# Optimization experiments

Hardware: AMD Instinct MI355X
Metric: run time of the kernel (lower is better)

The kernel has to match this reference:

```python
import jax, jax.numpy as jnp
import numpy as np

B, N, C, H, W = 4, 24, 256, 100, 100
SCALE = 0.25      # feature-map stride scale (MultiScaleRoIAlign spatial scale)
OUT = 7           # output_size
SR = 2            # sampling_ratio
IMG = H / SCALE   # image size in box coordinates (400)


def setup_inputs() -> dict:
    key = jax.random.key(0)
    kf, kx, ky, kw, kh = jax.random.split(key, 5)
    features = jax.random.normal(kf, (B, C, H, W), dtype=jnp.float32)
    # valid boxes: positive height/width (module asserts non-degenerate boxes)
    x1 = jax.random.uniform(kx, (B, N), minval=0.0, maxval=IMG * 0.6)
    y1 = jax.random.uniform(ky, (B, N), minval=0.0, maxval=IMG * 0.6)
    bw = jax.random.uniform(kw, (B, N), minval=16.0, maxval=IMG * 0.35)
    bh = jax.random.uniform(kh, (B, N), minval=16.0, maxval=IMG * 0.35)
    x2 = jnp.minimum(x1 + bw, IMG - 1.0)
    y2 = jnp.minimum(y1 + bh, IMG - 1.0)
    boxes = jnp.stack([x1, y1, x2, y2], axis=-1)  # [B, N, 4] xyxy
    return {"features": features, "boxes": boxes}


def _roi_align(features, rois, batch_ix):
    """torchvision-style RoIAlign (aligned=False). rois: [R,4] xyxy in image coords."""
    R = rois.shape[0]
    x1, y1, x2, y2 = [rois[:, i] * SCALE for i in range(4)]
    roi_w = jnp.maximum(x2 - x1, 1.0)
    roi_h = jnp.maximum(y2 - y1, 1.0)
    bin_w = roi_w / OUT
    bin_h = roi_h / OUT
    # sample-point offsets within the roi: (bin + (k+0.5)/SR) for k in [0,SR)
    grid = (jnp.arange(OUT, dtype=jnp.float32)[:, None]
            + (jnp.arange(SR, dtype=jnp.float32)[None, :] + 0.5) / SR).reshape(-1)  # [OUT*SR]
    ys = y1[:, None] + grid[None, :] * bin_h[:, None]  # [R, 14]
    xs = x1[:, None] + grid[None, :] * bin_w[:, None]  # [R, 14]
    Y = ys[:, :, None]  # [R,14,1]
    X = xs[:, None, :]  # [R,1,14]
    valid = (Y > -1.0) & (Y < H) & (X > -1.0) & (X < W)  # [R,14,14]
    Yc = jnp.clip(Y, 0.0, H - 1.0)
    Xc = jnp.clip(X, 0.0, W - 1.0)
    y0f = jnp.floor(Yc); x0f = jnp.floor(Xc)
    ly = Yc - y0f; lx = Xc - x0f
    hy = 1.0 - ly;  hx = 1.0 - lx
    y0 = y0f.astype(jnp.int32); x0 = x0f.astype(jnp.int32)
    y1i = jnp.minimum(y0 + 1, H - 1); x1i = jnp.minimum(x0 + 1, W - 1)
    b = batch_ix[:, None, None]
    # gathers -> [R,14,14,C] each (advanced indices around the ':' put C last)
    f00 = features[b, :, y0,  x0]
    f01 = features[b, :, y0,  x1i]
    f10 = features[b, :, y1i, x0]
    f11 = features[b, :, y1i, x1i]
    w00 = (hy * hx)[..., None]; w01 = (hy * lx)[..., None]
    w10 = (ly * hx)[..., None]; w11 = (ly * lx)[..., None]
    val = (w00 * f00 + w01 * f01 + w10 * f10 + w11 * f11) * valid[..., None]
    # average SRxSR samples per bin -> [R, OUT, OUT, C] -> [R, C, OUT, OUT]
    pooled = val.reshape(R, OUT, SR, OUT, SR, C).mean(axis=(2, 4))
    return pooled.transpose(0, 3, 1, 2)


def reference(features, boxes):
    # 1) pairwise union boxes (vectorized form of _single_image_expand)
    iu, ju = jnp.triu_indices(N, k=1)          # P pairs, i<j
    b1 = boxes[:, iu]                          # [B, P, 4]
    b2 = boxes[:, ju]
    union = jnp.concatenate([jnp.minimum(b1[..., :2], b2[..., :2]),
                             jnp.maximum(b1[..., 2:], b2[..., 2:])], axis=-1)
    rois = jnp.concatenate([boxes, union], axis=1)  # [B, M, 4], M = N + P
    M = rois.shape[1]
    batch_ix = jnp.repeat(jnp.arange(B), M)
    pooled = _roi_align(features, rois.reshape(-1, 4), batch_ix)  # [B*M, C, 7, 7]
    pooled = pooled.reshape(B, M, C, OUT, OUT)
    # 2) pair assembly (vectorized _ObjPairLayer): [obj_i, obj_j, union_ij]
    obj = pooled[:, :N]    # [B, N, C, 7, 7]
    uni = pooled[:, N:]    # [B, P, C, 7, 7]
    pair_feats = jnp.stack([obj[:, iu], obj[:, ju], uni], axis=2)  # [B, P, 3, C, 7, 7]
    P = iu.shape[0]
    return pair_feats.reshape(B * P, 3, C, OUT, OUT)
```

## Files before the change

### kernel.cpp

```cpp
#include <hip/hip_runtime.h>

#define B_    4
#define N_OBJ 24
#define C_    256
#define H_    100
#define W_    100
#define HW_   (H_ * W_)
#define OUT_  7
#define P_    276
#define M_    (N_OBJ + P_)
#define SCALE_ 0.25f
#define CHW_OUT (C_ * OUT_ * OUT_)

typedef float f4_t __attribute__((ext_vector_type(4)));

__global__ __launch_bounds__(256) void transpose_kernel(
        const float* __restrict__ feat, float* __restrict__ featT) {
    __shared__ float tile[64][65];
    const int b   = blockIdx.z;
    const int c0  = blockIdx.y * 64;
    const int px0 = blockIdx.x * 64;
    const int t   = threadIdx.x;
    const int cl  = t >> 6;
    const int px  = t & 63;
#pragma unroll
    for (int k = 0; k < 16; ++k) {
        const int c_loc = cl + k * 4;
        const int gpx   = px0 + px;
        tile[c_loc][px] = (gpx < HW_)
            ? feat[((size_t)b * C_ + c0 + c_loc) * HW_ + gpx] : 0.0f;
    }
    __syncthreads();
    const int c2 = t & 63;
    const int pl = t >> 6;
#pragma unroll
    for (int k = 0; k < 16; ++k) {
        const int px_l = pl + k * 4;
        const int gpx  = px0 + px_l;
        if (gpx < HW_)
            featT[((size_t)b * HW_ + gpx) * C_ + c0 + c2] = tile[c2][px_l];
    }
}

__global__ __launch_bounds__(256) void roi_fused_kernel(
        const float* __restrict__ featT,
        const float* __restrict__ boxes,
        float* __restrict__ out) {
    __shared__ float lds[CHW_OUT];
    const int blk    = blockIdx.x;
    const bool is_obj = blk < B_ * N_OBJ;
    int b, m;
    if (is_obj) {
        b = (blk & 7) >> 1;
        m = ((blk >> 3) << 1) | (blk & 1);
    } else {
        const int t = blk - B_ * N_OBJ;
        b = (t & 7) >> 1;
        m = N_OBJ + (((t >> 3) << 1) | (t & 1));
    }

    float x1, y1, x2, y2;
    if (is_obj) {
        const float* bp = boxes + ((size_t)b * N_OBJ + m) * 4;
        x1 = bp[0]; y1 = bp[1]; x2 = bp[2]; y2 = bp[3];
    } else {
        int p = m - N_OBJ;
        int ii = 0, rem = p;
        while (rem >= N_OBJ - 1 - ii) { rem -= (N_OBJ - 1 - ii); ++ii; }
        const int jj = ii + 1 + rem;
        const float* b1 = boxes + ((size_t)b * N_OBJ + ii) * 4;
        const float* b2 = boxes + ((size_t)b * N_OBJ + jj) * 4;
        x1 = fminf(b1[0], b2[0]); y1 = fminf(b1[1], b2[1]);
        x2 = fmaxf(b1[2], b2[2]); y2 = fmaxf(b1[3], b2[3]);
    }
    x1 *= SCALE_; y1 *= SCALE_; x2 *= SCALE_; y2 *= SCALE_;
    const float bin_w = fmaxf(x2 - x1, 1.0f) * (1.0f / OUT_);
    const float bin_h = fmaxf(y2 - y1, 1.0f) * (1.0f / OUT_);

    const int lane = threadIdx.x & 63;
    const int wv   = threadIdx.x >> 6;
    const f4_t* fbase = (const f4_t*)(featT + (size_t)b * HW_ * C_) + lane;

    for (int s = wv; s < OUT_ * OUT_; s += 4) {
        const int ph = s / OUT_, pw = s - ph * OUT_;

        int ri_[4]; float rw_[4];
        {
            const float Ya = y1 + ((float)ph + 0.25f) * bin_h;
            const float Yb = y1 + ((float)ph + 0.75f) * bin_h;
            const float va = (Ya > -1.0f && Ya < (float)H_) ? 1.0f : 0.0f;
            const float vb = (Yb > -1.0f && Yb < (float)H_) ? 1.0f : 0.0f;
            const float Yca = fminf(fmaxf(Ya, 0.0f), (float)(H_ - 1));
            const float Ycb = fminf(fmaxf(Yb, 0.0f), (float)(H_ - 1));
            const int y0a = (int)floorf(Yca);
            const int y0b = (int)floorf(Ycb);
            const float lya = Yca - (float)y0a;
            const float lyb = Ycb - (float)y0b;
            ri_[0] = y0a; ri_[1] = min(y0a + 1, H_ - 1);
            ri_[2] = y0b; ri_[3] = min(y0b + 1, H_ - 1);
            rw_[0] = va * (1.0f - lya); rw_[1] = va * lya;
            rw_[2] = vb * (1.0f - lyb); rw_[3] = vb * lyb;
            if (ri_[1] == ri_[0]) { rw_[0] += rw_[1]; rw_[1] = 0.0f; }
            if (ri_[3] == ri_[2]) { rw_[2] += rw_[3]; rw_[3] = 0.0f; }
            if (ri_[2] == ri_[0]) {
                rw_[0] += rw_[2]; rw_[1] += rw_[3]; rw_[2] = 0.0f; rw_[3] = 0.0f;
            } else if (ri_[2] == ri_[1]) {
                rw_[1] += rw_[2]; rw_[2] = 0.0f;
            }
        }
        int ci_[4]; float cw_[4];
        {
            const float Xa = x1 + ((float)pw + 0.25f) * bin_w;
            const float Xb = x1 + ((float)pw + 0.75f) * bin_w;
            const float va = (Xa > -1.0f && Xa < (float)W_) ? 0.25f : 0.0f;
            const float vb = (Xb > -1.0f && Xb < (float)W_) ? 0.25f : 0.0f;
            const float Xca = fminf(fmaxf(Xa, 0.0f), (float)(W_ - 1));
            const float Xcb = fminf(fmaxf(Xb, 0.0f), (float)(W_ - 1));
            const int x0a = (int)floorf(Xca);
            const int x0b = (int)floorf(Xcb);
            const float lxa = Xca - (float)x0a;
            const float lxb = Xcb - (float)x0b;
            ci_[0] = x0a; ci_[1] = min(x0a + 1, W_ - 1);
            ci_[2] = x0b; ci_[3] = min(x0b + 1, W_ - 1);
            cw_[0] = va * (1.0f - lxa); cw_[1] = va * lxa;
            cw_[2] = vb * (1.0f - lxb); cw_[3] = vb * lxb;
            if (ci_[1] == ci_[0]) { cw_[0] += cw_[1]; cw_[1] = 0.0f; }
            if (ci_[3] == ci_[2]) { cw_[2] += cw_[3]; cw_[3] = 0.0f; }
            if (ci_[2] == ci_[0]) {
                cw_[0] += cw_[2]; cw_[1] += cw_[3]; cw_[2] = 0.0f; cw_[3] = 0.0f;
            } else if (ci_[2] == ci_[1]) {
                cw_[1] += cw_[2]; cw_[2] = 0.0f;
            }
        }

        int   offs[16]; float wts[16];
#pragma unroll
        for (int r = 0; r < 4; ++r)
#pragma unroll
            for (int c = 0; c < 4; ++c) {
                offs[r * 4 + c] = (ri_[r] * W_ + ci_[c]) * (C_ / 4);
                wts[r * 4 + c]  = rw_[r] * cw_[c];
            }
        f4_t f[16];
#pragma unroll
        for (int k = 0; k < 16; ++k)
            if (wts[k] != 0.0f) f[k] = fbase[offs[k]];
        f4_t acc = (f4_t){0.f, 0.f, 0.f, 0.f};
#pragma unroll
        for (int k = 0; k < 16; ++k)
            if (wts[k] != 0.0f) acc += wts[k] * f[k];

        const int c0 = lane * 4;
        lds[(c0 + 0) * 49 + s] = acc.x;
        lds[(c0 + 1) * 49 + s] = acc.y;
        lds[(c0 + 2) * 49 + s] = acc.z;
        lds[(c0 + 3) * 49 + s] = acc.w;
    }
    __syncthreads();

    const f4_t* s4 = (const f4_t*)lds;
    if (!is_obj) {
        const int p = m - N_OBJ;
        f4_t* d4 = (f4_t*)(out + (((size_t)(b * P_ + p)) * 3 + 2) * CHW_OUT);
        for (int idx = threadIdx.x; idx < CHW_OUT / 4; idx += 256)
            __builtin_nontemporal_store(s4[idx], d4 + idx);
    } else {
        for (int q = 0; q < N_OBJ; ++q) {
            if (q == m) continue;
            const int i = min(m, q), j = max(m, q);
            const int p = i * (2 * N_OBJ - i - 1) / 2 + (j - i - 1);
            const int slot = (m < q) ? 0 : 1;
            f4_t* d4 = (f4_t*)(out + (((size_t)(b * P_ + p)) * 3 + slot) * CHW_OUT);
            for (int idx = threadIdx.x; idx < CHW_OUT / 4; idx += 256)
                __builtin_nontemporal_store(s4[idx], d4 + idx);
        }
    }
}

extern "C" void kernel_launch(void* const* d_in, const int* in_sizes, int n_in,
                              void* d_out, int out_size, void* d_ws, size_t ws_size,
                              hipStream_t stream) {
    const float* feat  = (const float*)d_in[0];
    const float* boxes = (const float*)d_in[1];
    float* out = (float*)d_out;

    float* featT = (float*)d_ws;

    transpose_kernel<<<dim3((HW_ + 63) / 64, C_ / 64, B_), 256, 0, stream>>>(feat, featT);
    roi_fused_kernel<<<B_ * M_, 256, 0, stream>>>(featT, boxes, out);
}
```

Before: 248.5 us.

## Split object pooling into separate kernel and assemble pair rows in union kernel

Object RoIs are now pooled by their own kernel into a workspace buffer. The union kernel then writes each output pair row as one contiguous 3-slot block, copying the two object features from the workspace. Before, each object block wrote 23 scattered copies itself, which left a few long-tail blocks. The cost is an extra kernel launch with a serial dependency, and workspace reads that should mostly hit L2.

```diff
diff --git a/kernel.cpp b/kernel.cpp
--- a/kernel.cpp
+++ b/kernel.cpp
@@ -8,7 +8,6 @@
 #define HW_   (H_ * W_)
 #define OUT_  7
 #define P_    276
-#define M_    (N_OBJ + P_)
 #define SCALE_ 0.25f
 #define CHW_OUT (C_ * OUT_ * OUT_)
 
@@ -42,44 +41,12 @@
     }
 }
 
-__global__ __launch_bounds__(256) void roi_fused_kernel(
-        const float* __restrict__ featT,
-        const float* __restrict__ boxes,
-        float* __restrict__ out) {
-    __shared__ float lds[CHW_OUT];
-    const int blk    = blockIdx.x;
-    const bool is_obj = blk < B_ * N_OBJ;
-    int b, m;
-    if (is_obj) {
-        b = (blk & 7) >> 1;
-        m = ((blk >> 3) << 1) | (blk & 1);
-    } else {
-        const int t = blk - B_ * N_OBJ;
-        b = (t & 7) >> 1;
-        m = N_OBJ + (((t >> 3) << 1) | (t & 1));
-    }
-
-    float x1, y1, x2, y2;
-    if (is_obj) {
-        const float* bp = boxes + ((size_t)b * N_OBJ + m) * 4;
-        x1 = bp[0]; y1 = bp[1]; x2 = bp[2]; y2 = bp[3];
-    } else {
-        int p = m - N_OBJ;
-        int ii = 0, rem = p;
-        while (rem >= N_OBJ - 1 - ii) { rem -= (N_OBJ - 1 - ii); ++ii; }
-        const int jj = ii + 1 + rem;
-        const float* b1 = boxes + ((size_t)b * N_OBJ + ii) * 4;
-        const float* b2 = boxes + ((size_t)b * N_OBJ + jj) * 4;
-        x1 = fminf(b1[0], b2[0]); y1 = fminf(b1[1], b2[1]);
-        x2 = fmaxf(b1[2], b2[2]); y2 = fmaxf(b1[3], b2[3]);
-    }
+__device__ __forceinline__ void pool_to_lds(
+        const f4_t* __restrict__ fbase, float x1, float y1, float x2, float y2,
+        float* __restrict__ lds, int lane, int wv) {
     x1 *= SCALE_; y1 *= SCALE_; x2 *= SCALE_; y2 *= SCALE_;
     const float bin_w = fmaxf(x2 - x1, 1.0f) * (1.0f / OUT_);
     const float bin_h = fmaxf(y2 - y1, 1.0f) * (1.0f / OUT_);
-
-    const int lane = threadIdx.x & 63;
-    const int wv   = threadIdx.x >> 6;
-    const f4_t* fbase = (const f4_t*)(featT + (size_t)b * HW_ * C_) + lane;
 
     for (int s = wv; s < OUT_ * OUT_; s += 4) {
         const int ph = s / OUT_, pw = s - ph * OUT_;
@@ -156,24 +123,62 @@
         lds[(c0 + 2) * 49 + s] = acc.z;
         lds[(c0 + 3) * 49 + s] = acc.w;
     }
+}
+
+__global__ __launch_bounds__(256) void obj_kernel(
+        const float* __restrict__ featT, const float* __restrict__ boxes,
+        float* __restrict__ ws_obj) {
+    __shared__ float lds[CHW_OUT];
+    const int blk = blockIdx.x;
+    const int b   = (blk & 7) >> 1;
+    const int m   = ((blk >> 3) << 1) | (blk & 1);
+
+    const float* bp = boxes + ((size_t)b * N_OBJ + m) * 4;
+    const int lane = threadIdx.x & 63;
+    const int wv   = threadIdx.x >> 6;
+    const f4_t* fbase = (const f4_t*)(featT + (size_t)b * HW_ * C_) + lane;
+    pool_to_lds(fbase, bp[0], bp[1], bp[2], bp[3], lds, lane, wv);
     __syncthreads();
 
     const f4_t* s4 = (const f4_t*)lds;
-    if (!is_obj) {
-        const int p = m - N_OBJ;
-        f4_t* d4 = (f4_t*)(out + (((size_t)(b * P_ + p)) * 3 + 2) * CHW_OUT);
-        for (int idx = threadIdx.x; idx < CHW_OUT / 4; idx += 256)
-            __builtin_nontemporal_store(s4[idx], d4 + idx);
-    } else {
-        for (int q = 0; q < N_OBJ; ++q) {
-            if (q == m) continue;
-            const int i = min(m, q), j = max(m, q);
-            const int p = i * (2 * N_OBJ - i - 1) / 2 + (j - i - 1);
-            const int slot = (m < q) ? 0 : 1;
-            f4_t* d4 = (f4_t*)(out + (((size_t)(b * P_ + p)) * 3 + slot) * CHW_OUT);
-            for (int idx = threadIdx.x; idx < CHW_OUT / 4; idx += 256)
-                __builtin_nontemporal_store(s4[idx], d4 + idx);
-        }
+    f4_t* d4 = (f4_t*)(ws_obj + ((size_t)b * N_OBJ + m) * CHW_OUT);
+    for (int idx = threadIdx.x; idx < CHW_OUT / 4; idx += 256)
+        d4[idx] = s4[idx];
+}
+
+__global__ __launch_bounds__(256) void union_kernel(
+        const float* __restrict__ featT, const float* __restrict__ boxes,
+        const float* __restrict__ ws_obj, float* __restrict__ out) {
+    __shared__ float lds[CHW_OUT];
+    const int blk = blockIdx.x;
+    const int b   = (blk & 7) >> 1;
+    const int p   = ((blk >> 3) << 1) | (blk & 1);
+
+    int ii = 0, rem = p;
+    while (rem >= N_OBJ - 1 - ii) { rem -= (N_OBJ - 1 - ii); ++ii; }
+    const int jj = ii + 1 + rem;
+    const float* b1 = boxes + ((size_t)b * N_OBJ + ii) * 4;
+    const float* b2 = boxes + ((size_t)b * N_OBJ + jj) * 4;
+    const float x1 = fminf(b1[0], b2[0]), y1 = fminf(b1[1], b2[1]);
+    const float x2 = fmaxf(b1[2], b2[2]), y2 = fmaxf(b1[3], b2[3]);
+
+    const int lane = threadIdx.x & 63;
+    const int wv   = threadIdx.x >> 6;
+    const f4_t* fbase = (const f4_t*)(featT + (size_t)b * HW_ * C_) + lane;
+    pool_to_lds(fbase, x1, y1, x2, y2, lds, lane, wv);
+    __syncthreads();
+
+    const f4_t* s4 = (const f4_t*)lds;
+    const f4_t* si = (const f4_t*)(ws_obj + ((size_t)b * N_OBJ + ii) * CHW_OUT);
+    const f4_t* sj = (const f4_t*)(ws_obj + ((size_t)b * N_OBJ + jj) * CHW_OUT);
+    f4_t* d4 = (f4_t*)(out + ((size_t)(b * P_ + p)) * 3 * CHW_OUT);
+    for (int idx = threadIdx.x; idx < CHW_OUT / 4; idx += 256) {
+        const f4_t v0 = si[idx];
+        const f4_t v1 = sj[idx];
+        const f4_t v2 = s4[idx];
+        __builtin_nontemporal_store(v0, d4 + idx);
+        __builtin_nontemporal_store(v1, d4 + (CHW_OUT / 4) + idx);
+        __builtin_nontemporal_store(v2, d4 + 2 * (CHW_OUT / 4) + idx);
     }
 }
 
@@ -184,8 +189,10 @@
     const float* boxes = (const float*)d_in[1];
     float* out = (float*)d_out;
 
-    float* featT = (float*)d_ws;
+    float* featT  = (float*)d_ws;
+    float* ws_obj = featT + (size_t)B_ * HW_ * C_;
 
     transpose_kernel<<<dim3((HW_ + 63) / 64, C_ / 64, B_), 256, 0, stream>>>(feat, featT);
-    roi_fused_kernel<<<B_ * M_, 256, 0, stream>>>(featT, boxes, out);
+    obj_kernel<<<B_ * N_OBJ, 256, 0, stream>>>(featT, boxes, ws_obj);
+    union_kernel<<<B_ * P_, 256, 0, stream>>>(featT, boxes, ws_obj, out);
 }
```

Result: slower. 269.3 us (+8.4%).
